# Kernel optimization log

Measured on AMD Instinct MI355X. Metric: run time of the kernel, lower is better.

The kernel has to match this reference:

```python
import jax, jax.numpy as jnp
import numpy as np
from jax import lax

IMG = 1024
STRIDES = (4, 8, 16, 32, 64)
SIZE_BASES = (32, 64, 128, 256, 512)
SCALES = (8.0,)
RATIOS = (0.5, 1.0, 2.0)
PRE_NMS = 2000
POST_NMS = 1000
NMS_THRESH = 0.7
B = 4


def _level_anchors(stride, size_base):
    """Anchors [G*G*A, 4] in xyxy, centered on grid cells."""
    g = IMG // stride
    cs = (jnp.arange(g, dtype=jnp.float32) + 0.5) * stride
    cy, cx = jnp.meshgrid(cs, cs, indexing='ij')          # [g,g]
    ctr = jnp.stack([cx.ravel(), cy.ravel()], axis=-1)    # [g*g, 2]
    wh = []
    for r in RATIOS:
        for s in SCALES:
            wh.append((size_base * s * np.sqrt(1.0 / r), size_base * s * np.sqrt(r)))
    wh = jnp.asarray(wh, jnp.float32)                     # [A, 2]
    x1y1 = ctr[:, None, :] - 0.5 * wh[None, :, :]
    x2y2 = ctr[:, None, :] + 0.5 * wh[None, :, :]
    return jnp.concatenate([x1y1, x2y2], axis=-1).reshape(-1, 4)


def _decode(anchors, deltas):
    wa = anchors[:, 2] - anchors[:, 0]
    ha = anchors[:, 3] - anchors[:, 1]
    cxa = anchors[:, 0] + 0.5 * wa
    cya = anchors[:, 1] + 0.5 * ha
    dx, dy, dw, dh = deltas[:, 0], deltas[:, 1], deltas[:, 2], deltas[:, 3]
    cx = dx * wa + cxa
    cy = dy * ha + cya
    w = jnp.exp(dw) * wa
    h = jnp.exp(dh) * ha
    return jnp.stack([cx - 0.5 * w, cy - 0.5 * h, cx + 0.5 * w, cy + 0.5 * h], axis=-1)


def _clip(boxes, info):
    h, w = info[0], info[1]
    x = jnp.clip(boxes[:, 0::2], 0.0, w - 1.0)
    y = jnp.clip(boxes[:, 1::2], 0.0, h - 1.0)
    return jnp.stack([x[:, 0], y[:, 0], x[:, 1], y[:, 1]], axis=-1)


def _iou_matrix(boxes):
    area = jnp.maximum(boxes[:, 2] - boxes[:, 0], 0.0) * jnp.maximum(boxes[:, 3] - boxes[:, 1], 0.0)
    lt = jnp.maximum(boxes[:, None, :2], boxes[None, :, :2])
    rb = jnp.minimum(boxes[:, None, 2:], boxes[None, :, 2:])
    wh = jnp.maximum(rb - lt, 0.0)
    inter = wh[..., 0] * wh[..., 1]
    return inter / jnp.maximum(area[:, None] + area[None, :] - inter, 1e-9)


def _nms_keep(boxes, thresh):
    """Boxes sorted by score desc. Returns boolean keep mask."""
    iou = _iou_matrix(boxes)
    n = boxes.shape[0]
    idx = jnp.arange(n)
    def body(i, keep):
        sup = keep[i] & (iou[i] > thresh) & (idx > i)
        return keep & ~sup
    return lax.fori_loop(0, n, body, jnp.ones((n,), bool))


def reference(probs0, probs1, probs2, probs3, probs4,
              reg0, reg1, reg2, reg3, reg4, img_info):
    anchors = [_level_anchors(s, b) for s, b in zip(STRIDES, SIZE_BASES)]
    probs = (probs0, probs1, probs2, probs3, probs4)
    regs = (reg0, reg1, reg2, reg3, reg4)

    def per_image(pr, rg, info):
        boxes_all, scores_all = [], []
        for a, p, r in zip(anchors, pr, rg):
            scores = p[:, 0]
            proposals = _clip(_decode(a, r), info)
            k = min(PRE_NMS, scores.shape[0])
            s, order = lax.top_k(scores, k)        # pre-NMS top-k, sorted desc
            bx = proposals[order]
            keep = _nms_keep(bx, NMS_THRESH)
            s = jnp.where(keep, s, -1.0)           # suppressed -> sentinel
            kp = min(POST_NMS, k)
            s2, o2 = lax.top_k(s, kp)              # post-NMS top-k per level
            boxes_all.append(bx[o2])
            scores_all.append(s2)
        ab = jnp.concatenate(boxes_all, axis=0)
        asc = jnp.concatenate(scores_all, axis=0)
        fs, fo = lax.top_k(asc, POST_NMS)          # merge levels, final top-k
        fb = jnp.where((fs >= 0.0)[:, None], ab[fo], 0.0)  # zero-pad invalid
        return fb

    fb = jax.vmap(per_image)(probs, regs, img_info)        # [B, POST, 4]
    bidx = jnp.broadcast_to(jnp.arange(B, dtype=fb.dtype)[:, None, None], (B, POST_NMS, 1))
    return jnp.concatenate([bidx, fb], axis=-1)            # [B, POST, 5]


def setup_inputs():
    key = jax.random.key(0)
    ks = jax.random.split(key, 10)
    grids = [IMG // s for s in STRIDES]
    A = [g * g * len(RATIOS) * len(SCALES) for g in grids]
    inp = {}
    for l in range(5):
        inp[f'probs{l}'] = jax.random.uniform(ks[l], (B, A[l], 2), dtype=jnp.float32)
        inp[f'reg{l}'] = 0.1 * jax.random.normal(ks[5 + l], (B, A[l], 4), dtype=jnp.float32)
    inp['img_info'] = jnp.tile(jnp.array([IMG, IMG, 1.0], jnp.float32), (B, 1))
    return inp
```

## Files before the change

### kernel.cpp

```cpp
#include <hip/hip_runtime.h>
#include <stdint.h>
#include <math.h>

#pragma clang fp contract(off)

#define NB 4
#define TOTA 261888
#define PRE 2000
#define POST 1000
#define CATN 4768
#define NBL 20
#define CANDCAP 4096
#define NBLK 4092
#define BPB 1023
#define HBLK 65

__device__ __forceinline__ unsigned keyF(float f) {
  unsigned u = __float_as_uint(f);
  return (u & 0x80000000u) ? ~u : (u | 0x80000000u);
}

__device__ __forceinline__ int lvlA(int l)   { switch (l) { case 0: return 196608; case 1: return 49152; case 2: return 12288; case 3: return 3072; default: return 768; } }
__device__ __forceinline__ int lvlOff(int l) { switch (l) { case 0: return 0; case 1: return 196608; case 2: return 245760; case 3: return 258048; default: return 261120; } }
__device__ __forceinline__ int lvlK(int l)   { return l == 4 ? 768 : 2000; }
__device__ __forceinline__ int lvlKP(int l)  { return l == 4 ? 768 : 1000; }
__device__ __forceinline__ int lvlBlkStart(int l) { switch (l) { case 0: return 0; case 1: return 768; case 2: return 960; case 3: return 1008; default: return 1020; } }
__device__ __forceinline__ int lvlBlkCnt(int l)   { switch (l) { case 0: return 768; case 1: return 192; case 2: return 48; case 3: return 12; default: return 3; } }

struct InPtrs {
  const float *p0, *p1, *p2, *p3, *p4;
  const float *r0, *r1, *r2, *r3, *r4;
  const float *info;
};

__device__ __forceinline__ void gaToLvl(int ga, int& l, int& off) {
  if (ga < 196608)      { l = 0; off = 0; }
  else if (ga < 245760) { l = 1; off = 196608; }
  else if (ga < 258048) { l = 2; off = 245760; }
  else if (ga < 261120) { l = 3; off = 258048; }
  else                  { l = 4; off = 261120; }
}

__device__ __forceinline__ void fatMap(int s, int& l, int& seg) {
  if (s < 48)      { l = 0; seg = s; }
  else if (s < 60) { l = 1; seg = s - 48; }
  else if (s < 63) { l = 2; seg = s - 60; }
  else if (s == 63){ l = 3; seg = 0; }
  else             { l = 4; seg = 0; }
}

__global__ __launch_bounds__(256) void k_decode(InPtrs P, float4* __restrict__ props,
                                                float* __restrict__ scores) {
  int gid = blockIdx.x * 256 + threadIdx.x;
  if (gid >= NB * TOTA) return;
  int b = gid / TOTA, ga = gid % TOTA;
  int Al, off, lg; float st; double S; const float *prp, *rgp;
  if (ga < 196608)      { Al = 196608; off = 0;      lg = 8; st = 4.0f;  S = 256.0;  prp = P.p0; rgp = P.r0; }
  else if (ga < 245760) { Al = 49152;  off = 196608; lg = 7; st = 8.0f;  S = 512.0;  prp = P.p1; rgp = P.r1; }
  else if (ga < 258048) { Al = 12288;  off = 245760; lg = 6; st = 16.0f; S = 1024.0; prp = P.p2; rgp = P.r2; }
  else if (ga < 261120) { Al = 3072;   off = 258048; lg = 5; st = 32.0f; S = 2048.0; prp = P.p3; rgp = P.r3; }
  else                  { Al = 768;    off = 261120; lg = 4; st = 64.0f; S = 4096.0; prp = P.p4; rgp = P.r4; }
  int i = ga - off;
  int cell = i / 3, rr = i - cell * 3;
  int col = cell & ((1 << lg) - 1), row = cell >> lg;
  float cx0 = ((float)col + 0.5f) * st;
  float cy0 = ((float)row + 0.5f) * st;
  const double SQ2 = 1.4142135623730951;
  const double SQH = 0.7071067811865476;
  double swd = (rr == 0) ? SQ2 : (rr == 1 ? 1.0 : SQH);
  double shd = (rr == 0) ? SQH : (rr == 1 ? 1.0 : SQ2);
  float wf = (float)(S * swd), hf = (float)(S * shd);
  float ax1 = cx0 - 0.5f * wf, ay1 = cy0 - 0.5f * hf;
  float ax2 = cx0 + 0.5f * wf, ay2 = cy0 + 0.5f * hf;
  size_t base = (size_t)b * Al + i;
  float sc = prp[base * 2];
  float4 d4 = ((const float4*)rgp)[base];
  float dx = d4.x, dy = d4.y, dw = d4.z, dh = d4.w;
  float wa = ax2 - ax1, ha = ay2 - ay1;
  float cxa = ax1 + 0.5f * wa, cya = ay1 + 0.5f * ha;
  float cx = dx * wa + cxa, cy = dy * ha + cya;
  float w = (float)exp((double)dw) * wa;
  float h = (float)exp((double)dh) * ha;
  float x1 = cx - 0.5f * w, y1 = cy - 0.5f * h;
  float x2 = cx + 0.5f * w, y2 = cy + 0.5f * h;
  float Hc = P.info[b * 3 + 0] - 1.0f, Wc = P.info[b * 3 + 1] - 1.0f;
  float4 o;
  o.x = fminf(fmaxf(x1, 0.0f), Wc);
  o.y = fminf(fmaxf(y1, 0.0f), Hc);
  o.z = fminf(fmaxf(x2, 0.0f), Wc);
  o.w = fminf(fmaxf(y2, 0.0f), Hc);
  props[gid] = o;
  scores[gid] = sc;
}

__global__ __launch_bounds__(256) void k_hist8(const float* __restrict__ scores,
                                               unsigned* __restrict__ hist8) {
  __shared__ unsigned h[256];
  int blk = blockIdx.x;
  int b = blk / HBLK, s = blk % HBLK;
  int l, seg; fatMap(s, l, seg);
  int n = lvlA(l), off = lvlOff(l);
  int start = seg * 4096;
  int cnt_s = min(4096, n - start);
  int tid = threadIdx.x;
  h[tid] = 0;
  __syncthreads();
  const float* sc = scores + (size_t)b * TOTA + off + start;
  for (int q = tid; q < cnt_s; q += 256)
    atomicAdd(&h[keyF(sc[q]) >> 24], 1u);
  __syncthreads();
  unsigned v = h[tid];
  if (v) atomicAdd(&hist8[(b * 5 + l) * 256 + tid], v);
}

__global__ __launch_bounds__(256) void k_thr8(const unsigned* __restrict__ hist8,
                                              unsigned* __restrict__ c1r1) {
  __shared__ unsigned h[256];
  int bl = blockIdx.x, tid = threadIdx.x;
  h[tid] = hist8[bl * 256 + tid];
  __syncthreads();
  if (tid == 0) {
    unsigned K = (unsigned)lvlK(bl % 5), cum = 0; int c;
    for (c = 255; c > 0; --c) { if (cum + h[c] >= K) break; cum += h[c]; }
    c1r1[bl * 2] = (unsigned)c;
    c1r1[bl * 2 + 1] = K - cum;
  }
}

__global__ __launch_bounds__(256) void k_hist6(const float* __restrict__ scores,
                                               const unsigned* __restrict__ c1r1,
                                               unsigned* __restrict__ hist6) {
  __shared__ unsigned h[64];
  int blk = blockIdx.x;
  int b = blk / HBLK, s = blk % HBLK;
  int l, seg; fatMap(s, l, seg);
  int n = lvlA(l), off = lvlOff(l);
  int start = seg * 4096;
  int cnt_s = min(4096, n - start);
  int tid = threadIdx.x;
  int bl = b * 5 + l;
  unsigned c1 = c1r1[bl * 2];
  if (tid < 64) h[tid] = 0;
  __syncthreads();
  const float* sc = scores + (size_t)b * TOTA + off + start;
  for (int q = tid; q < cnt_s; q += 256) {
    unsigned key = keyF(sc[q]);
    if ((key >> 24) == c1) atomicAdd(&h[(key >> 18) & 63u], 1u);
  }
  __syncthreads();
  if (tid < 64) {
    unsigned v = h[tid];
    if (v) atomicAdd(&hist6[bl * 64 + tid], v);
  }
}

__global__ __launch_bounds__(64) void k_thr6(const unsigned* __restrict__ hist6,
                                             const unsigned* __restrict__ c1r1,
                                             unsigned* __restrict__ T14) {
  __shared__ unsigned h[64];
  int bl = blockIdx.x, tid = threadIdx.x;
  h[tid] = hist6[bl * 64 + tid];
  __syncthreads();
  if (tid == 0) {
    unsigned r1 = c1r1[bl * 2 + 1], cum = 0; int c;
    for (c = 63; c > 0; --c) { if (cum + h[c] >= r1) break; cum += h[c]; }
    T14[bl] = (c1r1[bl * 2] << 6) | (unsigned)c;
  }
}

__global__ __launch_bounds__(256) void k_cnt(const float* __restrict__ scores,
                                             const unsigned* __restrict__ T14,
                                             unsigned* __restrict__ blockCnt) {
  __shared__ unsigned ws[4];
  int gid = blockIdx.x * 256 + threadIdx.x;
  int tid = threadIdx.x;
  int b = gid / TOTA, ga = gid % TOTA;
  int l, off; gaToLvl(ga, l, off);
  int bl = b * 5 + l;
  bool pred = (keyF(scores[gid]) >> 18) >= T14[bl];
  unsigned long long m = __ballot(pred);
  if ((tid & 63) == 0) ws[tid >> 6] = (unsigned)__popcll(m);
  __syncthreads();
  if (tid == 0) blockCnt[blockIdx.x] = ws[0] + ws[1] + ws[2] + ws[3];
}

__global__ __launch_bounds__(1024) void k_scanblk(const unsigned* __restrict__ blockCnt,
                                                  unsigned* __restrict__ blockBase,
                                                  unsigned* __restrict__ cnt) {
  __shared__ unsigned a[4096];
  __shared__ unsigned ch[1024];
  int tid = threadIdx.x;
  int q0 = tid * 4;
  unsigned a0 = (q0 + 0 < NBLK) ? blockCnt[q0 + 0] : 0u;
  unsigned a1 = (q0 + 1 < NBLK) ? blockCnt[q0 + 1] : 0u;
  unsigned a2 = (q0 + 2 < NBLK) ? blockCnt[q0 + 2] : 0u;
  unsigned a3 = (q0 + 3 < NBLK) ? blockCnt[q0 + 3] : 0u;
  unsigned p0 = a0, p1 = p0 + a1, p2 = p1 + a2, p3 = p2 + a3;
  ch[tid] = p3;
  __syncthreads();
  for (int d = 1; d < 1024; d <<= 1) {
    unsigned t = (tid >= d) ? ch[tid - d] : 0u;
    __syncthreads();
    ch[tid] += t;
    __syncthreads();
  }
  unsigned cbase = (tid > 0) ? ch[tid - 1] : 0u;
  a[q0 + 0] = cbase + p0;
  a[q0 + 1] = cbase + p1;
  a[q0 + 2] = cbase + p2;
  a[q0 + 3] = cbase + p3;
  __syncthreads();
  for (int k = 0; k < 4; ++k) {
    int g = q0 + k;
    if (g < NBLK) {
      int b = g / BPB, r = g % BPB;
      int l = (r < 768) ? 0 : (r < 960) ? 1 : (r < 1008) ? 2 : (r < 1020) ? 3 : 4;
      int ss = b * BPB + lvlBlkStart(l);
      unsigned Eg = (g > 0) ? a[g - 1] : 0u;
      unsigned Es = (ss > 0) ? a[ss - 1] : 0u;
      blockBase[g] = Eg - Es;
    }
  }
  if (tid < NBL) {
    int b = tid / 5, l = tid % 5;
    int ss = b * BPB + lvlBlkStart(l);
    int ee = ss + lvlBlkCnt(l);
    unsigned Ee = a[ee - 1];
    unsigned Es = (ss > 0) ? a[ss - 1] : 0u;
    cnt[tid] = Ee - Es;
  }
}

__global__ __launch_bounds__(256) void k_fill(const float* __restrict__ scores,
                                              const unsigned* __restrict__ T14,
                                              const unsigned* __restrict__ blockBase,
                                              unsigned long long* __restrict__ cand) {
  __shared__ unsigned ws[4];
  int gid = blockIdx.x * 256 + threadIdx.x;
  int tid = threadIdx.x;
  int b = gid / TOTA, ga = gid % TOTA;
  int l, off; gaToLvl(ga, l, off);
  int bl = b * 5 + l;
  unsigned key = keyF(scores[gid]);
  bool pred = (key >> 18) >= T14[bl];
  unsigned long long m = __ballot(pred);
  int wv = tid >> 6, ln = tid & 63;
  if (ln == 0) ws[wv] = (unsigned)__popcll(m);
  __syncthreads();
  unsigned wo = 0;
  for (int q = 0; q < wv; ++q) wo += ws[q];
  unsigned pre = (unsigned)__popcll(m & ((1ull << ln) - 1ull));
  if (pred) {
    unsigned p = blockBase[blockIdx.x] + wo + pre;
    if (p < CANDCAP)
      cand[(size_t)bl * CANDCAP + p] =
          ((unsigned long long)key << 32) | (unsigned long long)(0xFFFFFFFFu - (unsigned)(ga - off));
  }
}

__global__ __launch_bounds__(256) void k_sortc(unsigned long long* __restrict__ cand,
                                               const unsigned* __restrict__ cnt) {
  __shared__ unsigned long long arr[512];
  int blk = blockIdx.x;
  int bl = blk >> 3, ch = blk & 7;
  int base = ch * 512;
  int num = (int)min(cnt[bl], (unsigned)CANDCAP);
  int tid = threadIdx.x;
  unsigned long long* cp = cand + (size_t)bl * CANDCAP + base;
  for (int q = tid; q < 512; q += 256)
    arr[q] = (base + q < num) ? cp[q] : 0ull;
  __syncthreads();
  for (int kk = 2; kk <= 512; kk <<= 1)
    for (int jj = kk >> 1; jj > 0; jj >>= 1) {
      for (int idx = tid; idx < 512; idx += 256) {
        int p2 = idx ^ jj;
        if (p2 > idx) {
          unsigned long long x = arr[idx], y = arr[p2];
          bool up = (idx & kk) == 0;
          if (up ? (x < y) : (x > y)) { arr[idx] = y; arr[p2] = x; }
        }
      }
      __syncthreads();
    }
  for (int q = tid; q < 512; q += 256) cp[q] = arr[q];
}

__global__ __launch_bounds__(256) void k_rank(const unsigned long long* __restrict__ cand,
                                              const float4* __restrict__ props,
                                              const float* __restrict__ scores,
                                              float4* __restrict__ sBox,
                                              float* __restrict__ sArea,
                                              float* __restrict__ sScore) {
  int gid = blockIdx.x * 256 + threadIdx.x;
  int bl = gid >> 12, p = gid & 4095;
  int b = bl / 5, l = bl % 5;
  int K = lvlK(l), off = lvlOff(l);
  const unsigned long long* cp = cand + (size_t)bl * CANDCAP;
  unsigned long long me = cp[p];
  int ch = p >> 9;
  int rank = p & 511;
  for (int c2 = 0; c2 < 8; ++c2) {
    if (c2 == ch) continue;
    const unsigned long long* d = cp + c2 * 512;
    int lo = 0, hi = 512;
    while (lo < hi) {
      int mid = (lo + hi) >> 1;
      if (d[mid] > me) lo = mid + 1; else hi = mid;
    }
    rank += lo;
  }
  if (rank < K) {
    unsigned idx = 0xFFFFFFFFu - (unsigned)(me & 0xFFFFFFFFull);
    float4 bx = props[(size_t)b * TOTA + off + idx];
    float area = fmaxf(bx.z - bx.x, 0.0f) * fmaxf(bx.w - bx.y, 0.0f);
    sBox[bl * PRE + rank] = bx;
    sArea[bl * PRE + rank] = area;
    sScore[bl * PRE + rank] = scores[(size_t)b * TOTA + off + idx];
  }
}

__global__ __launch_bounds__(256) void k_mask(const float4* __restrict__ sBox,
                                              const float* __restrict__ sArea,
                                              unsigned long long* __restrict__ mask) {
  int bi = blockIdx.x;
  int bl = bi >> 8, rem = bi & 255, ic = rem >> 3, wc = rem & 7;
  int l = bl % 5, K = lvlK(l);
  if (ic * 64 >= K) return;
  int tid = threadIdx.x;
  int j0 = wc * 256;
  int iL = tid >> 2, wL = tid & 3;
  int i = ic * 64 + iL;
  if (j0 + 255 <= ic * 64) {
    if (i < K) mask[((size_t)bl * PRE + i) * 32 + (wc * 4 + wL)] = 0ull;
    return;
  }
  __shared__ float4 jb[256];
  __shared__ float ja[256];
  {
    int j = j0 + tid;
    if (j < K) { jb[tid] = sBox[bl * PRE + j]; ja[tid] = sArea[bl * PRE + j]; }
    else { jb[tid] = make_float4(0.0f, 0.0f, 0.0f, 0.0f); ja[tid] = 0.0f; }
  }
  __syncthreads();
  if (i >= K) return;
  float4 a4 = sBox[bl * PRE + i];
  float ai = sArea[bl * PRE + i];
  unsigned long long bits = 0;
  int tb = wL * 64;
  for (int t = 0; t < 64; ++t) {
    int j = j0 + tb + t;
    if (j < K && j > i) {
      float4 b4 = jb[tb + t];
      float ltx = fmaxf(a4.x, b4.x), lty = fmaxf(a4.y, b4.y);
      float rbx = fminf(a4.z, b4.z), rby = fminf(a4.w, b4.w);
      float wx = fmaxf(rbx - ltx, 0.0f), wy = fmaxf(rby - lty, 0.0f);
      float inter = wx * wy;
      float den = fmaxf(ai + ja[tb + t] - inter, 1e-9f);
      float iou = inter / den;
      if (iou > 0.7f) bits |= (1ull << t);
    }
  }
  mask[((size_t)bl * PRE + i) * 32 + (wc * 4 + wL)] = bits;
}

__global__ __launch_bounds__(1024) void k_nms(const unsigned long long* __restrict__ mask,
                                              const float4* __restrict__ sBox,
                                              const float* __restrict__ sScore,
                                              float* __restrict__ catScore,
                                              float4* __restrict__ catBox) {
  __shared__ unsigned long long diag[PRE];
  __shared__ unsigned long long remv[32];
  __shared__ int list[1000];
  __shared__ int sTotal;
  int bl = blockIdx.x, b = bl / 5, l = bl % 5;
  int K = lvlK(l), KP = lvlKP(l), co = l * 1000;
  int tid = threadIdx.x;
  const unsigned long long* mrow = mask + (size_t)bl * PRE * 32;
  int c = tid & 31, g = tid >> 5;
  int nw = (K + 63) >> 6;
  for (int r = tid; r < K; r += 1024) diag[r] = mrow[(size_t)r * 32 + (r >> 6)];
  if (tid < 32) remv[tid] = 0ull;
  __syncthreads();
  unsigned long long w0 = 0ull, w1 = 0ull, nw0 = 0ull, nw1 = 0ull;
  {
    bool act = (c > 0) && (c < nw);
    int row0 = g, row1 = g + 32;
    if (act && row0 < K) w0 = mrow[(size_t)row0 * 32 + c];
    if (act && row1 < K) w1 = mrow[(size_t)row1 * 32 + c];
  }
  for (int t = 0; t < nw; ++t) {
    nw0 = 0ull; nw1 = 0ull;
    if (t + 1 < nw) {
      bool actn = (c > t + 1) && (c < nw);
      int row0 = (t + 1) * 64 + g, row1 = row0 + 32;
      if (actn && row0 < K) nw0 = mrow[(size_t)row0 * 32 + c];
      if (actn && row1 < K) nw1 = mrow[(size_t)row1 * 32 + c];
    }
    if (tid < 64) {
      int dr = t * 64 + tid;
      unsigned long long d = (dr < K) ? diag[dr] : 0ull;
      unsigned long long local = remv[t];
      int lim = min(64, K - t * 64);
      unsigned long long validm = (lim >= 64) ? ~0ull : ((1ull << lim) - 1ull);
      unsigned long long todo = (~local) & validm;
      while (todo) {
        int i2 = __ffsll((long long)todo) - 1;
        unsigned lo2 = __builtin_amdgcn_readlane((unsigned)d, i2);
        unsigned hi2 = __builtin_amdgcn_readlane((unsigned)(d >> 32), i2);
        unsigned long long dd = ((unsigned long long)hi2 << 32) | (unsigned long long)lo2;
        local |= dd;
        todo &= ~dd;
        todo &= ~(1ull << i2);
      }
      if (tid == 0) remv[t] = local;
    }
    __syncthreads();
    {
      unsigned long long local = remv[t];
      bool act = (c > t) && (c < nw);
      if (act) {
        unsigned long long acc = 0ull;
        int row0 = t * 64 + g, row1 = row0 + 32;
        if (row0 < K && !((local >> g) & 1ull)) acc |= w0;
        if (row1 < K && !((local >> (g + 32)) & 1ull)) acc |= w1;
        if (acc) atomicOr(&remv[c], acc);
      }
    }
    __syncthreads();
    w0 = nw0; w1 = nw1;
  }
  if (tid < 64) {
    int lane = tid;
    bool lv = lane < 32;
    unsigned long long remw = lv ? remv[lane] : 0ull;
    unsigned long long valid = 0ull;
    if (lv) {
      int rem = K - lane * 64;
      valid = (rem >= 64) ? ~0ull : (rem <= 0 ? 0ull : ((1ull << rem) - 1ull));
    }
    unsigned long long keepw = (~remw) & valid;
    unsigned long long suppw = remw & valid;
    unsigned long long lmask = (1ull << lane) - 1ull;
    int base = 0;
    for (int w2 = 0; w2 < 32 && base < KP; ++w2) {
      unsigned long long word = __shfl(keepw, w2);
      int pre = __popcll(word & lmask);
      if (((word >> lane) & 1ull) && (base + pre) < KP) list[base + pre] = w2 * 64 + lane;
      base += __popcll(word);
    }
    int totalKept = base;
    if (totalKept < KP) {
      int b2 = totalKept;
      for (int w2 = 0; w2 < 32 && b2 < KP; ++w2) {
        unsigned long long word = __shfl(suppw, w2);
        int pre = __popcll(word & lmask);
        if (((word >> lane) & 1ull) && (b2 + pre) < KP) list[b2 + pre] = w2 * 64 + lane;
        b2 += __popcll(word);
      }
    }
    if (lane == 0) sTotal = totalKept;
  }
  __syncthreads();
  int totalKept = sTotal;
  for (int t = tid; t < KP; t += 1024) {
    int j = list[t];
    float s = (t < totalKept) ? sScore[bl * PRE + j] : -1.0f;
    catScore[b * CATN + co + t] = s;
    catBox[b * CATN + co + t] = sBox[bl * PRE + j];
  }
}

__global__ __launch_bounds__(256) void k_final(const float* __restrict__ catScore,
                                               const float4* __restrict__ catBox,
                                               float* __restrict__ out) {
  int gid = blockIdx.x * 256 + threadIdx.x;
  if (gid >= NB * CATN) return;
  int b = gid / CATN, p = gid % CATN;
  int c = p / 1000; if (c > 4) c = 4;
  const float* cs = catScore + (size_t)b * CATN;
  float s = cs[p];
  unsigned long long me = ((unsigned long long)keyF(s) << 32) |
                          (unsigned long long)(0xFFFFFFFFu - (unsigned)p);
  int rank = p - c * 1000;
  for (int c2 = 0; c2 < 5; ++c2) {
    if (c2 == c) continue;
    int base = c2 * 1000, len = (c2 == 4) ? 768 : 1000;
    int lo = 0, hi = len;
    while (lo < hi) {
      int mid = (lo + hi) >> 1;
      int q = base + mid;
      unsigned long long k2 = ((unsigned long long)keyF(cs[q]) << 32) |
                              (unsigned long long)(0xFFFFFFFFu - (unsigned)q);
      if (k2 > me) lo = mid + 1; else hi = mid;
    }
    rank += lo;
  }
  if (rank < POST) {
    float4 bx = make_float4(0.0f, 0.0f, 0.0f, 0.0f);
    if (s >= 0.0f) bx = catBox[(size_t)b * CATN + p];
    float* o = out + ((size_t)b * POST + rank) * 5;
    o[0] = (float)b; o[1] = bx.x; o[2] = bx.y; o[3] = bx.z; o[4] = bx.w;
  }
}

extern "C" void kernel_launch(void* const* d_in, const int* in_sizes, int n_in,
                              void* d_out, int out_size, void* d_ws, size_t ws_size,
                              hipStream_t stream) {
  const int prSz[5] = {1572864, 393216, 98304, 24576, 6144};
  const int rgSz[5] = {3145728, 786432, 196608, 49152, 12288};
  const float* pr[5] = {nullptr, nullptr, nullptr, nullptr, nullptr};
  const float* rg[5] = {nullptr, nullptr, nullptr, nullptr, nullptr};
  const float* info = nullptr;
  for (int i = 0; i < n_in; ++i) {
    int s = in_sizes[i];
    bool m = false;
    for (int l = 0; l < 5; ++l) {
      if (s == prSz[l]) { pr[l] = (const float*)d_in[i]; m = true; break; }
      if (s == rgSz[l]) { rg[l] = (const float*)d_in[i]; m = true; break; }
    }
    if (!m && s == 12) info = (const float*)d_in[i];
  }
  InPtrs P;
  P.p0 = pr[0]; P.p1 = pr[1]; P.p2 = pr[2]; P.p3 = pr[3]; P.p4 = pr[4];
  P.r0 = rg[0]; P.r1 = rg[1]; P.r2 = rg[2]; P.r3 = rg[3]; P.r4 = rg[4];
  P.info = info;

  char* w = (char*)d_ws;
  float4* props = (float4*)w;                         w += (size_t)NB * TOTA * 16;
  float4* sBox = (float4*)w;                          w += (size_t)NBL * PRE * 16;
  float4* catBox = (float4*)w;                        w += (size_t)NB * CATN * 16;
  unsigned long long* mask = (unsigned long long*)w;  w += (size_t)NBL * PRE * 32 * 8;
  unsigned long long* cand = (unsigned long long*)w;  w += (size_t)NBL * CANDCAP * 8;
  float* scores = (float*)w;                          w += (size_t)NB * TOTA * 4;
  float* sArea = (float*)w;                           w += (size_t)NBL * PRE * 4;
  float* sScore = (float*)w;                          w += (size_t)NBL * PRE * 4;
  float* catScore = (float*)w;                        w += (size_t)NB * CATN * 4;
  unsigned* hist8 = (unsigned*)w;                     w += (size_t)NBL * 256 * 4;
  unsigned* hist6 = (unsigned*)w;                     w += (size_t)NBL * 64 * 4;
  unsigned* c1r1 = (unsigned*)w;                      w += (size_t)NBL * 2 * 4;
  unsigned* T14 = (unsigned*)w;                       w += (size_t)NBL * 4;
  unsigned* blockCnt = (unsigned*)w;                  w += (size_t)NBLK * 4;
  unsigned* blockBase = (unsigned*)w;                 w += (size_t)NBLK * 4;
  unsigned* cnt = (unsigned*)w;                       w += (size_t)NBL * 4;
  (void)ws_size; (void)out_size;

  hipMemsetAsync(hist8, 0, (size_t)NBL * (256 + 64) * 4, stream);

  k_decode<<<(NB * TOTA + 255) / 256, 256, 0, stream>>>(P, props, scores);
  k_hist8<<<NB * HBLK, 256, 0, stream>>>(scores, hist8);
  k_thr8<<<NBL, 256, 0, stream>>>(hist8, c1r1);
  k_hist6<<<NB * HBLK, 256, 0, stream>>>(scores, c1r1, hist6);
  k_thr6<<<NBL, 64, 0, stream>>>(hist6, c1r1, T14);
  k_cnt<<<NBLK, 256, 0, stream>>>(scores, T14, blockCnt);
  k_scanblk<<<1, 1024, 0, stream>>>(blockCnt, blockBase, cnt);
  k_fill<<<NBLK, 256, 0, stream>>>(scores, T14, blockBase, cand);
  k_sortc<<<NBL * 8, 256, 0, stream>>>(cand, cnt);
  k_rank<<<NBL * CANDCAP / 256, 256, 0, stream>>>(cand, props, scores, sBox, sArea, sScore);
  k_mask<<<NBL * 256, 256, 0, stream>>>(sBox, sArea, mask);
  k_nms<<<NBL, 1024, 0, stream>>>(mask, sBox, sScore, catScore, catBox);
  k_final<<<(NB * CATN + 255) / 256, 256, 0, stream>>>(catScore, catBox, (float*)d_out);
}
```

Measured before the change: 206.9 us.

## Retile NMS IoU mask kernel to 256x256 tiles with one row per thread

The IoU mask kernel now uses 256x256 (i,j) tiles, one i-row per thread covering all four 64-bit words of the j-tile, instead of 64-row chunks with four threads per row. Grid size drops fourfold and tiles strictly below the diagonal are skipped. Off-diagonal tiles take a branch-free path with no j>i test. Zero-filling of lower-triangle words is dropped on the assumption that the NMS kernel never reads them. Each thread does four times more serial work, so there is less parallelism per block.

```diff
diff --git a/kernel.cpp b/kernel.cpp
--- a/kernel.cpp
+++ b/kernel.cpp
@@ -323,44 +323,67 @@
                                               const float* __restrict__ sArea,
                                               unsigned long long* __restrict__ mask) {
   int bi = blockIdx.x;
-  int bl = bi >> 8, rem = bi & 255, ic = rem >> 3, wc = rem & 7;
+  int bl = bi >> 6, rem2 = bi & 63, s = rem2 >> 3, jc = rem2 & 7;
   int l = bl % 5, K = lvlK(l);
-  if (ic * 64 >= K) return;
-  int tid = threadIdx.x;
-  int j0 = wc * 256;
-  int iL = tid >> 2, wL = tid & 3;
-  int i = ic * 64 + iL;
-  if (j0 + 255 <= ic * 64) {
-    if (i < K) mask[((size_t)bl * PRE + i) * 32 + (wc * 4 + wL)] = 0ull;
-    return;
-  }
+  int i0 = s * 256, j0 = jc * 256;
+  if (i0 >= K || j0 >= K) return;
+  if (jc < s) return;
+  int tid = threadIdx.x;
   __shared__ float4 jb[256];
   __shared__ float ja[256];
-  {
-    int j = j0 + tid;
-    if (j < K) { jb[tid] = sBox[bl * PRE + j]; ja[tid] = sArea[bl * PRE + j]; }
-    else { jb[tid] = make_float4(0.0f, 0.0f, 0.0f, 0.0f); ja[tid] = 0.0f; }
-  }
-  __syncthreads();
-  if (i >= K) return;
-  float4 a4 = sBox[bl * PRE + i];
-  float ai = sArea[bl * PRE + i];
-  unsigned long long bits = 0;
-  int tb = wL * 64;
-  for (int t = 0; t < 64; ++t) {
-    int j = j0 + tb + t;
-    if (j < K && j > i) {
-      float4 b4 = jb[tb + t];
-      float ltx = fmaxf(a4.x, b4.x), lty = fmaxf(a4.y, b4.y);
-      float rbx = fminf(a4.z, b4.z), rby = fminf(a4.w, b4.w);
-      float wx = fmaxf(rbx - ltx, 0.0f), wy = fmaxf(rby - lty, 0.0f);
-      float inter = wx * wy;
-      float den = fmaxf(ai + ja[tb + t] - inter, 1e-9f);
-      float iou = inter / den;
-      if (iou > 0.7f) bits |= (1ull << t);
-    }
-  }
-  mask[((size_t)bl * PRE + i) * 32 + (wc * 4 + wL)] = bits;
+  int jend = min(256, K - j0);
+  if (tid < jend) { jb[tid] = sBox[bl * PRE + j0 + tid]; ja[tid] = sArea[bl * PRE + j0 + tid]; }
+  int i = i0 + tid;
+  bool iv = i < K;
+  float4 bi4 = make_float4(0.0f, 0.0f, 0.0f, 0.0f);
+  float ai = 0.0f;
+  if (iv) { bi4 = sBox[bl * PRE + i]; ai = sArea[bl * PRE + i]; }
+  __syncthreads();
+  bool mixed = (jc == s);
+  int nwords = (jend + 63) >> 6;
+  for (int wq = 0; wq < 4; ++wq) {
+    if (wq >= nwords) break;
+    int jbase = wq * 64;
+    int lim = min(64, jend - jbase);
+    unsigned long long wacc = 0ull;
+    if (mixed) {
+#pragma unroll 4
+      for (int t = 0; t < lim; ++t) {
+        float4 b4 = jb[jbase + t];
+        float aj = ja[jbase + t];
+        int j = j0 + jbase + t;
+        bool pred = false;
+        if (iv && j > i) {
+          float ltx = fmaxf(bi4.x, b4.x), lty = fmaxf(bi4.y, b4.y);
+          float rbx = fminf(bi4.z, b4.z), rby = fminf(bi4.w, b4.w);
+          float wx = fmaxf(rbx - ltx, 0.0f), wy = fmaxf(rby - lty, 0.0f);
+          float inter = wx * wy;
+          float den = fmaxf(ai + aj - inter, 1e-9f);
+          pred = (inter / den) > 0.7f;
+        }
+        wacc |= ((unsigned long long)(pred ? 1u : 0u)) << t;
+      }
+    } else {
+#pragma unroll 4
+      for (int t = 0; t < lim; ++t) {
+        float4 b4 = jb[jbase + t];
+        float aj = ja[jbase + t];
+        bool pred = false;
+        if (iv) {
+          float ltx = fmaxf(bi4.x, b4.x), lty = fmaxf(bi4.y, b4.y);
+          float rbx = fminf(bi4.z, b4.z), rby = fminf(bi4.w, b4.w);
+          float wx = fmaxf(rbx - ltx, 0.0f), wy = fmaxf(rby - lty, 0.0f);
+          float inter = wx * wy;
+          float den = fmaxf(ai + aj - inter, 1e-9f);
+          pred = (inter / den) > 0.7f;
+        }
+        wacc |= ((unsigned long long)(pred ? 1u : 0u)) << t;
+      }
+    }
+    int jw = jc * 4 + wq;
+    if (iv && jw >= (i >> 6))
+      mask[((size_t)bl * PRE + i) * 32 + jw] = wacc;
+  }
 }
 
 __global__ __launch_bounds__(1024) void k_nms(const unsigned long long* __restrict__ mask,
@@ -556,7 +579,7 @@
   k_fill<<<NBLK, 256, 0, stream>>>(scores, T14, blockBase, cand);
   k_sortc<<<NBL * 8, 256, 0, stream>>>(cand, cnt);
   k_rank<<<NBL * CANDCAP / 256, 256, 0, stream>>>(cand, props, scores, sBox, sArea, sScore);
-  k_mask<<<NBL * 256, 256, 0, stream>>>(sBox, sArea, mask);
+  k_mask<<<NBL * 64, 256, 0, stream>>>(sBox, sArea, mask);
   k_nms<<<NBL, 1024, 0, stream>>>(mask, sBox, sScore, catScore, catBox);
   k_final<<<(NB * CATN + 255) / 256, 256, 0, stream>>>(catScore, catBox, (float*)d_out);
 }
```

New measurement: 218.5 us. 5.6% more time.
